# Kernel tuning notes

Hardware: AMD Instinct MI355X
Metric: run time of the kernel (lower is better)

The kernel has to match this reference:

```python
import jax, jax.numpy as jnp
import numpy as np


def setup_inputs() -> dict:
    key = jax.random.key(0)
    k1, k2, k3, k4, k5 = jax.random.split(key, 5)
    B, K, S, E, I, D = 4, 2, 512, 8, 1024, 2048
    x = jax.random.normal(k1, (B, S, I), dtype=jnp.float32)
    weights = jax.random.uniform(k2, (B, K, S), dtype=jnp.float32)
    ensembles = jax.random.randint(k3, (B, K, S), 0, E, dtype=jnp.int64)
    # xavier_uniform-style init for expert weight tables
    lim1 = float(np.sqrt(6.0 / (D + I)))
    proj_in = jax.random.uniform(k4, (E, D, I), dtype=jnp.float32, minval=-lim1, maxval=lim1)
    proj_out = jax.random.uniform(k5, (E, I, D), dtype=jnp.float32, minval=-lim1, maxval=lim1)
    return {"x": x, "weights": weights, "ensembles": ensembles,
            "proj_in": proj_in, "proj_out": proj_out}


def reference(x, weights, ensembles, proj_in, proj_out):
    # x: (B,S,I); weights/ensembles: (B,K,S); proj_in: (E,D,I); proj_out: (E,I,D)
    # Same math as the torch module (dropout = identity in eval):
    #   per token t, out = sum_k w[k,t] * W2[e_kt] @ relu(W1[e_kt] @ x[t])
    # Computed as all-expert batched GEMMs + a gated (one-hot scatter) combine,
    # which is mathematically identical and avoids the (B,K,S,D,I) gather blowup.
    E = proj_in.shape[0]
    h = jax.nn.relu(jnp.einsum('edi,bsi->bsed', proj_in, x))      # (B,S,E,D)
    o = jnp.einsum('eid,bsed->bsei', proj_out, h)                 # (B,S,E,I)
    onehot = jax.nn.one_hot(ensembles, E, dtype=x.dtype)          # (B,K,S,E)
    gate = jnp.einsum('bks,bkse->bse', weights, onehot)           # (B,S,E)
    return jnp.einsum('bsei,bse->bsi', o, gate)                   # (B,S,I)
```

## Files before the change

### kernel.cpp

```cpp
#include <hip/hip_runtime.h>
#include <stdint.h>

#define THREADS 512
#define BM 256
#define BN 128
#define BK 64
#define MAXT 24
#define NE 8
#define BB 4
#define SS 512
#define KK 2
#define II 1024
#define DD 2048
#define NTOK (BB * SS)
#define NASSIGN (BB * KK * SS)

#define CH_X (NTOK * II / 8)
#define CH_P (NE * DD * II / 8)
#define CB_X (CH_X / 256)
#define CB_P (CH_P / 256)
#define CB_TOTAL (CB_X + 2 * CB_P)

typedef unsigned short u16;
typedef __attribute__((ext_vector_type(8))) __bf16 bf16x8;
typedef __attribute__((ext_vector_type(4))) float f32x4;
typedef __attribute__((ext_vector_type(4))) unsigned int u32x4;

__device__ __forceinline__ u16 f32_to_bf16(float f) {
    unsigned int u = __builtin_bit_cast(unsigned int, f);
    unsigned int r = u + 0x7FFFu + ((u >> 16) & 1u);
    return (u16)(r >> 16);
}

__device__ __forceinline__ void gload16(const void* g, void* l) {
    __builtin_amdgcn_global_load_lds(
        (const __attribute__((address_space(1))) unsigned int*)g,
        (__attribute__((address_space(3))) unsigned int*)l, 16, 0, 0);
}

__global__ void setup_kernel(const void* __restrict__ ens_raw,
                             const float* __restrict__ weights,
                             int* __restrict__ meta,
                             int* __restrict__ tok,
                             float* __restrict__ wgt) {
    __shared__ int s_cnt[NE];
    __shared__ int s_cur[NE];
    __shared__ int s_flag;
    const int t = threadIdx.x;
    if (t < NE) s_cnt[t] = 0;
    if (t == 0) s_flag = 0;
    __syncthreads();

    const unsigned int* w32 = (const unsigned int*)ens_raw;
    unsigned int f = 0;
    for (int i = t; i < NASSIGN / 2; i += 256) f |= w32[2 * i + 1];
    if (f) atomicOr(&s_flag, 1);
    __syncthreads();
    const bool is32 = (s_flag != 0);
    const int* e32 = (const int*)ens_raw;
    const long long* e64 = (const long long*)ens_raw;

    for (int a = t; a < NASSIGN; a += 256) {
        int e = is32 ? e32[a] : (int)e64[a];
        atomicAdd(&s_cnt[e & 7], 1);
    }
    __syncthreads();

    if (t == 0) {
        int pb = 0, nt = 0;
        for (int e = 0; e < NE; e++) {
            int c = s_cnt[e];
            meta[8 + e] = c;
            meta[16 + e] = pb;
            s_cur[e] = pb;
            int n128 = (c + 127) >> 7;
            int pe = pb + n128 * 128;
            for (int i2 = 0; i2 < n128; i2 += 2) {
                meta[32 + nt] = e;
                meta[64 + nt] = pb + i2 * 128;
                meta[96 + nt] = pb + c;
                meta[128 + nt] = pe;
                nt++;
            }
            pb = pe;
        }
        meta[0] = nt;
        meta[1] = pb;
    }
    __syncthreads();

    for (int a = t; a < NASSIGN; a += 256) {
        int e = is32 ? e32[a] : (int)e64[a];
        e &= 7;
        int slot = atomicAdd(&s_cur[e], 1);
        int b = a >> 10;
        int s = a & (SS - 1);
        tok[slot] = b * SS + s;
        wgt[slot] = weights[a];
    }
    __syncthreads();

    for (int e = 0; e < NE; e++) {
        int st = meta[16 + e] + meta[8 + e];
        int en = (e < NE - 1) ? meta[16 + e + 1] : meta[1];
        for (int i = st + t; i < en; i += 256) {
            tok[i] = 0;
            wgt[i] = 0.f;
        }
    }
}

__global__ __launch_bounds__(256)
void convert3(const float* __restrict__ x,
              const float* __restrict__ pin,
              const float* __restrict__ pout,
              u16* __restrict__ xb,
              u16* __restrict__ pb1,
              u16* __restrict__ pb2) {
    const int b = blockIdx.x;
    const float* s;
    u16* d;
    int base;
    if (b < CB_X)            { s = x;    d = xb;  base = b << 8; }
    else if (b < CB_X + CB_P){ s = pin;  d = pb1; base = (b - CB_X) << 8; }
    else                     { s = pout; d = pb2; base = (b - CB_X - CB_P) << 8; }
    const size_t k = (size_t)base + threadIdx.x;
    const f32x4* s4 = (const f32x4*)s;
    f32x4 a = __builtin_nontemporal_load(&s4[2 * k]);
    f32x4 c = __builtin_nontemporal_load(&s4[2 * k + 1]);
    union { u16 u[8]; u32x4 v; } o;
    o.u[0] = f32_to_bf16(a[0]); o.u[1] = f32_to_bf16(a[1]);
    o.u[2] = f32_to_bf16(a[2]); o.u[3] = f32_to_bf16(a[3]);
    o.u[4] = f32_to_bf16(c[0]); o.u[5] = f32_to_bf16(c[1]);
    o.u[6] = f32_to_bf16(c[2]); o.u[7] = f32_to_bf16(c[3]);
    *(u32x4*)(d + 8 * k) = o.v;
}

template <int MODE>
__global__ __launch_bounds__(THREADS, 2)
void gemm256(const u16* __restrict__ Abase,
             const u16* __restrict__ Bbase,
             const int* __restrict__ meta,
             const int* __restrict__ tok,
             const float* __restrict__ wgt,
             u16* __restrict__ hdst,
             float* __restrict__ outdst) {
    constexpr int Kdim = (MODE == 0) ? II : DD;
    constexpr int NT = Kdim / BK;
    __shared__ char smem[3 * 49152];

    const int lid = blockIdx.x;
    const int g = lid & 7;
    const int i = lid >> 3;
    const int tile = g * 3 + (i % 3);
    const int colt = i / 3;
    if (tile >= meta[0]) return;

    const int e     = meta[32 + tile];
    const int sbase = meta[64 + tile];
    const int rend  = meta[96 + tile];
    const int wend  = meta[128 + tile];
    const int padmax = meta[1];
    const int colbase = colt * BN;

    const int tid = threadIdx.x;
    const int lane = tid & 63;
    const int wv = tid >> 6;
    const int wr = wv >> 1;
    const int wc = wv & 1;

    const u16* Bp = Bbase + (size_t)e * (size_t)(DD * II) + (size_t)colbase * Kdim;

    int aoff[4], boff[2], adst[4], bdst[2];
#pragma unroll
    for (int j = 0; j < 4; j++) {
        int c = j * 512 + tid;
        int row = c >> 3;
        int s = (c & 7) ^ (row & 7);
        adst[j] = c * 16;
        int slot = sbase + row;
        if (slot > padmax - 1) slot = padmax - 1;
        aoff[j] = (MODE == 0 ? tok[slot] * II : slot * DD) + s * 8;
    }
#pragma unroll
    for (int j = 0; j < 2; j++) {
        int c = j * 512 + tid;
        int row = c >> 3;
        int s = (c & 7) ^ (row & 7);
        bdst[j] = c * 16;
        boff[j] = row * Kdim + s * 8;
    }

    f32x4 acc[4][4];
#pragma unroll
    for (int m = 0; m < 4; m++)
#pragma unroll
        for (int n = 0; n < 4; n++)
            acc[m][n] = (f32x4){0.f, 0.f, 0.f, 0.f};

    auto STAGE = [&](int kt, char* buf) {
        const int kof = kt * BK;
#pragma unroll
        for (int j = 0; j < 4; j++)
            gload16(Abase + aoff[j] + kof, buf + adst[j]);
#pragma unroll
        for (int j = 0; j < 2; j++)
            gload16(Bp + boff[j] + kof, buf + 32768 + bdst[j]);
    };

    auto COMPUTE = [&](const char* buf) {
        const u16* As = (const u16*)buf;
        const u16* Bs = (const u16*)(buf + 32768);
        bf16x8 a[2][4], b[2][4];
#pragma unroll
        for (int kk = 0; kk < 2; kk++) {
#pragma unroll
            for (int m = 0; m < 4; m++) {
                int row = wr * 64 + m * 16 + (lane & 15);
                int slot = (kk * 4 + (lane >> 4)) ^ (row & 7);
                a[kk][m] = *(const bf16x8*)&As[row * 64 + slot * 8];
            }
#pragma unroll
            for (int n = 0; n < 4; n++) {
                int col = wc * 64 + n * 16 + (lane & 15);
                int slot = (kk * 4 + (lane >> 4)) ^ (col & 7);
                b[kk][n] = *(const bf16x8*)&Bs[col * 64 + slot * 8];
            }
        }
        __builtin_amdgcn_s_setprio(1);
#pragma unroll
        for (int m = 0; m < 4; m++)
#pragma unroll
            for (int n = 0; n < 4; n++) {
                acc[m][n] = __builtin_amdgcn_mfma_f32_16x16x32_bf16(
                    a[0][m], b[0][n], acc[m][n], 0, 0, 0);
                acc[m][n] = __builtin_amdgcn_mfma_f32_16x16x32_bf16(
                    a[1][m], b[1][n], acc[m][n], 0, 0, 0);
            }
        __builtin_amdgcn_s_setprio(0);
    };

    char* pA = smem;
    char* pB = smem + 49152;
    char* pC = smem + 98304;

    STAGE(0, pA);
    STAGE(1, pB);
    asm volatile("s_waitcnt vmcnt(6)" ::: "memory");
    __builtin_amdgcn_sched_barrier(0);
    __builtin_amdgcn_s_barrier();
    __builtin_amdgcn_sched_barrier(0);

#pragma unroll 1
    for (int t = 0; t < NT; ++t) {
        if (t + 2 < NT) STAGE(t + 2, pC);
        COMPUTE(pA);
        if (t + 2 < NT) {
            asm volatile("s_waitcnt vmcnt(6)" ::: "memory");
        } else if (t + 1 < NT) {
            asm volatile("s_waitcnt vmcnt(0)" ::: "memory");
        }
        __builtin_amdgcn_sched_barrier(0);
        __builtin_amdgcn_s_barrier();
        __builtin_amdgcn_sched_barrier(0);
        char* tmp = pA; pA = pB; pB = pC; pC = tmp;
    }

    if (MODE == 0) {
#pragma unroll
        for (int m = 0; m < 4; m++) {
#pragma unroll
            for (int r = 0; r < 4; r++) {
                int row = wr * 64 + m * 16 + (lane >> 4) * 4 + r;
                int slot = sbase + row;
                if (slot < wend) {
                    size_t ro = (size_t)slot * DD;
#pragma unroll
                    for (int n = 0; n < 4; n++) {
                        int col = colbase + wc * 64 + n * 16 + (lane & 15);
                        float v = acc[m][n][r];
                        v = v > 0.f ? v : 0.f;
                        hdst[ro + col] = f32_to_bf16(v);
                    }
                }
            }
        }
    } else {
#pragma unroll
        for (int m = 0; m < 4; m++) {
#pragma unroll
            for (int r = 0; r < 4; r++) {
                int row = wr * 64 + m * 16 + (lane >> 4) * 4 + r;
                int slot = sbase + row;
                if (slot < rend) {
                    float w = wgt[slot];
                    size_t obase = (size_t)tok[slot] * II;
#pragma unroll
                    for (int n = 0; n < 4; n++) {
                        int col = colbase + wc * 64 + n * 16 + (lane & 15);
                        atomicAdd(&outdst[obase + col], acc[m][n][r] * w);
                    }
                }
            }
        }
    }
}

extern "C" void kernel_launch(void* const* d_in, const int* in_sizes, int n_in,
                              void* d_out, int out_size, void* d_ws, size_t ws_size,
                              hipStream_t stream) {
    const float* x = (const float*)d_in[0];
    const float* weights = (const float*)d_in[1];
    const void* ens = d_in[2];
    const float* pin = (const float*)d_in[3];
    const float* pout = (const float*)d_in[4];
    float* out = (float*)d_out;

    char* ws = (char*)d_ws;
    int*   meta    = (int*)(ws);
    int*   tok     = (int*)(ws + 1024);
    float* wgt     = (float*)(ws + 21504);
    u16*   x_bf    = (u16*)(ws + 41984);
    u16*   pin_bf  = (u16*)(ws + 4236288);
    u16*   pout_bf = (u16*)(ws + 37790720);
    u16*   h       = (u16*)(ws + 71345152);

    setup_kernel<<<dim3(1), dim3(256), 0, stream>>>(ens, weights, meta, tok, wgt);

    hipMemsetAsync(d_out, 0, (size_t)out_size * sizeof(float), stream);

    convert3<<<dim3(CB_TOTAL), dim3(256), 0, stream>>>(x, pin, pout, x_bf, pin_bf, pout_bf);

    gemm256<0><<<dim3(8 * 3 * 16), dim3(THREADS), 0, stream>>>(
        x_bf, pin_bf, meta, tok, wgt, h, nullptr);

    gemm256<1><<<dim3(8 * 3 * 8), dim3(THREADS), 0, stream>>>(
        h, pout_bf, meta, tok, wgt, nullptr, out);
}
```

Baseline: 134.8 us.

## Fuse fp32-to-bf16 weight conversion into GEMM B-tile loads via registers

Drops the separate pass that converted both expert weight tables to bf16. The GEMMs now read the fp32 weights directly into registers, pack them with v_cvt_pk_bf16_f32, and write them into a double-buffered LDS B tile, with the main loop unrolled by two to alternate register sets. This removes a full read and write of about 134MB of weight data, but each GEMM block now fetches twice the bytes for B, and the same weight tile is re-read and re-converted by every tile that uses that expert. The tile-to-block mapping is also changed so that tiles for the same column share a block group.

```diff
diff --git a/kernel.cpp b/kernel.cpp
--- a/kernel.cpp
+++ b/kernel.cpp
@@ -5,7 +5,6 @@
 #define BM 256
 #define BN 128
 #define BK 64
-#define MAXT 24
 #define NE 8
 #define BB 4
 #define SS 512
@@ -16,10 +15,7 @@
 #define NASSIGN (BB * KK * SS)
 
 #define CH_X (NTOK * II / 8)
-#define CH_P (NE * DD * II / 8)
 #define CB_X (CH_X / 256)
-#define CB_P (CH_P / 256)
-#define CB_TOTAL (CB_X + 2 * CB_P)
 
 typedef unsigned short u16;
 typedef __attribute__((ext_vector_type(8))) __bf16 bf16x8;
@@ -32,11 +28,23 @@
     return (u16)(r >> 16);
 }
 
+__device__ __forceinline__ unsigned int cvtpk(float lo, float hi) {
+    unsigned int r;
+    asm("v_cvt_pk_bf16_f32 %0, %1, %2" : "=v"(r) : "v"(lo), "v"(hi));
+    return r;
+}
+
 __device__ __forceinline__ void gload16(const void* g, void* l) {
     __builtin_amdgcn_global_load_lds(
         (const __attribute__((address_space(1))) unsigned int*)g,
         (__attribute__((address_space(3))) unsigned int*)l, 16, 0, 0);
 }
+
+#define SYNC() do { \
+    asm volatile("s_waitcnt lgkmcnt(0)" ::: "memory"); \
+    __builtin_amdgcn_sched_barrier(0); \
+    __builtin_amdgcn_s_barrier(); \
+    __builtin_amdgcn_sched_barrier(0); } while (0)
 
 __global__ void setup_kernel(const void* __restrict__ ens_raw,
                              const float* __restrict__ weights,
@@ -111,21 +119,9 @@
 }
 
 __global__ __launch_bounds__(256)
-void convert3(const float* __restrict__ x,
-              const float* __restrict__ pin,
-              const float* __restrict__ pout,
-              u16* __restrict__ xb,
-              u16* __restrict__ pb1,
-              u16* __restrict__ pb2) {
-    const int b = blockIdx.x;
-    const float* s;
-    u16* d;
-    int base;
-    if (b < CB_X)            { s = x;    d = xb;  base = b << 8; }
-    else if (b < CB_X + CB_P){ s = pin;  d = pb1; base = (b - CB_X) << 8; }
-    else                     { s = pout; d = pb2; base = (b - CB_X - CB_P) << 8; }
-    const size_t k = (size_t)base + threadIdx.x;
-    const f32x4* s4 = (const f32x4*)s;
+void convertX(const float* __restrict__ x, u16* __restrict__ xb) {
+    const size_t k = (size_t)blockIdx.x * 256 + threadIdx.x;
+    const f32x4* s4 = (const f32x4*)x;
     f32x4 a = __builtin_nontemporal_load(&s4[2 * k]);
     f32x4 c = __builtin_nontemporal_load(&s4[2 * k + 1]);
     union { u16 u[8]; u32x4 v; } o;
@@ -133,13 +129,13 @@
     o.u[2] = f32_to_bf16(a[2]); o.u[3] = f32_to_bf16(a[3]);
     o.u[4] = f32_to_bf16(c[0]); o.u[5] = f32_to_bf16(c[1]);
     o.u[6] = f32_to_bf16(c[2]); o.u[7] = f32_to_bf16(c[3]);
-    *(u32x4*)(d + 8 * k) = o.v;
+    *(u32x4*)(xb + 8 * k) = o.v;
 }
 
 template <int MODE>
 __global__ __launch_bounds__(THREADS, 2)
 void gemm256(const u16* __restrict__ Abase,
-             const u16* __restrict__ Bbase,
+             const float* __restrict__ Bbase,
              const int* __restrict__ meta,
              const int* __restrict__ tok,
              const float* __restrict__ wgt,
@@ -147,19 +143,21 @@
              float* __restrict__ outdst) {
     constexpr int Kdim = (MODE == 0) ? II : DD;
     constexpr int NT = Kdim / BK;
-    __shared__ char smem[3 * 49152];
+    constexpr int ASZ = BM * BK * 2;
+    constexpr int BSZ = BN * BK * 2;
+    __shared__ char smem[3 * ASZ + 2 * BSZ];
 
     const int lid = blockIdx.x;
     const int g = lid & 7;
     const int i = lid >> 3;
-    const int tile = g * 3 + (i % 3);
+    const int tile = g + 8 * (i % 3);
     const int colt = i / 3;
     if (tile >= meta[0]) return;
 
-    const int e     = meta[32 + tile];
-    const int sbase = meta[64 + tile];
-    const int rend  = meta[96 + tile];
-    const int wend  = meta[128 + tile];
+    const int e      = meta[32 + tile];
+    const int sbase  = meta[64 + tile];
+    const int rend   = meta[96 + tile];
+    const int wend   = meta[128 + tile];
     const int padmax = meta[1];
     const int colbase = colt * BN;
 
@@ -169,9 +167,9 @@
     const int wr = wv >> 1;
     const int wc = wv & 1;
 
-    const u16* Bp = Bbase + (size_t)e * (size_t)(DD * II) + (size_t)colbase * Kdim;
-
-    int aoff[4], boff[2], adst[4], bdst[2];
+    const float* Bp32 = Bbase + (size_t)e * (size_t)(DD * II) + (size_t)colbase * Kdim;
+
+    int aoff[4], adst[4];
 #pragma unroll
     for (int j = 0; j < 4; j++) {
         int c = j * 512 + tid;
@@ -182,13 +180,15 @@
         if (slot > padmax - 1) slot = padmax - 1;
         aoff[j] = (MODE == 0 ? tok[slot] * II : slot * DD) + s * 8;
     }
+
+    int bsrc[2], bdst[2];
 #pragma unroll
     for (int j = 0; j < 2; j++) {
-        int c = j * 512 + tid;
-        int row = c >> 3;
-        int s = (c & 7) ^ (row & 7);
-        bdst[j] = c * 16;
-        boff[j] = row * Kdim + s * 8;
+        int c = 2 * tid + j;
+        int col = c >> 3;
+        int s0 = c & 7;
+        bsrc[j] = col * Kdim + s0 * 8;
+        bdst[j] = col * 128 + ((s0 ^ (col & 7)) * 16);
     }
 
     f32x4 acc[4][4];
@@ -198,19 +198,40 @@
         for (int n = 0; n < 4; n++)
             acc[m][n] = (f32x4){0.f, 0.f, 0.f, 0.f};
 
-    auto STAGE = [&](int kt, char* buf) {
+    f32x4 rE[2][2], rO[2][2];
+
+    auto STAGE_A = [&](int kt, char* buf) {
         const int kof = kt * BK;
 #pragma unroll
         for (int j = 0; j < 4; j++)
             gload16(Abase + aoff[j] + kof, buf + adst[j]);
-#pragma unroll
-        for (int j = 0; j < 2; j++)
-            gload16(Bp + boff[j] + kof, buf + 32768 + bdst[j]);
     };
 
-    auto COMPUTE = [&](const char* buf) {
-        const u16* As = (const u16*)buf;
-        const u16* Bs = (const u16*)(buf + 32768);
+    auto LOADB = [&](int kt, f32x4 (&R)[2][2]) {
+        const int kof = kt * BK;
+#pragma unroll
+        for (int j = 0; j < 2; j++) {
+            const f32x4* p = (const f32x4*)(Bp32 + bsrc[j] + kof);
+            R[j][0] = p[0];
+            R[j][1] = p[1];
+        }
+    };
+
+    auto WRITEB = [&](f32x4 (&R)[2][2], char* pbl) {
+#pragma unroll
+        for (int j = 0; j < 2; j++) {
+            u32x4 w;
+            w[0] = cvtpk(R[j][0][0], R[j][0][1]);
+            w[1] = cvtpk(R[j][0][2], R[j][0][3]);
+            w[2] = cvtpk(R[j][1][0], R[j][1][1]);
+            w[3] = cvtpk(R[j][1][2], R[j][1][3]);
+            *(u32x4*)(pbl + bdst[j]) = w;
+        }
+    };
+
+    auto COMPUTE = [&](const char* bufA, const char* bufB) {
+        const u16* As = (const u16*)bufA;
+        const u16* Bs = (const u16*)bufB;
         bf16x8 a[2][4], b[2][4];
 #pragma unroll
         for (int kk = 0; kk < 2; kk++) {
@@ -241,29 +262,31 @@
     };
 
     char* pA = smem;
-    char* pB = smem + 49152;
-    char* pC = smem + 98304;
-
-    STAGE(0, pA);
-    STAGE(1, pB);
-    asm volatile("s_waitcnt vmcnt(6)" ::: "memory");
+    char* pB = smem + ASZ;
+    char* pC = smem + 2 * ASZ;
+    char* pB0 = smem + 3 * ASZ;
+    char* pB1 = pB0 + BSZ;
+
+    STAGE_A(0, pA); LOADB(0, rE);
+    STAGE_A(1, pB); LOADB(1, rO);
     __builtin_amdgcn_sched_barrier(0);
-    __builtin_amdgcn_s_barrier();
-    __builtin_amdgcn_sched_barrier(0);
+    WRITEB(rE, pB0);
+    SYNC();
 
 #pragma unroll 1
-    for (int t = 0; t < NT; ++t) {
-        if (t + 2 < NT) STAGE(t + 2, pC);
-        COMPUTE(pA);
-        if (t + 2 < NT) {
-            asm volatile("s_waitcnt vmcnt(6)" ::: "memory");
-        } else if (t + 1 < NT) {
-            asm volatile("s_waitcnt vmcnt(0)" ::: "memory");
-        }
+    for (int t = 0; t < NT; t += 2) {
+        if (t + 2 < NT) { STAGE_A(t + 2, pC); LOADB(t + 2, rE); }
         __builtin_amdgcn_sched_barrier(0);
-        __builtin_amdgcn_s_barrier();
+        if (t + 1 < NT) WRITEB(rO, pB1);
+        COMPUTE(pA, pB0);
+        SYNC();
+        { char* tp = pA; pA = pB; pB = pC; pC = tp; }
+        if (t + 3 < NT) { STAGE_A(t + 3, pC); LOADB(t + 3, rO); }
         __builtin_amdgcn_sched_barrier(0);
-        char* tmp = pA; pA = pB; pB = pC; pC = tmp;
+        if (t + 2 < NT) WRITEB(rE, pB0);
+        COMPUTE(pA, pB1);
+        SYNC();
+        { char* tp = pA; pA = pB; pB = pC; pC = tp; }
     }
 
     if (MODE == 0) {
@@ -317,23 +340,21 @@
     float* out = (float*)d_out;
 
     char* ws = (char*)d_ws;
-    int*   meta    = (int*)(ws);
-    int*   tok     = (int*)(ws + 1024);
-    float* wgt     = (float*)(ws + 21504);
-    u16*   x_bf    = (u16*)(ws + 41984);
-    u16*   pin_bf  = (u16*)(ws + 4236288);
-    u16*   pout_bf = (u16*)(ws + 37790720);
-    u16*   h       = (u16*)(ws + 71345152);
+    int*   meta = (int*)(ws);
+    int*   tok  = (int*)(ws + 1024);
+    float* wgt  = (float*)(ws + 21504);
+    u16*   x_bf = (u16*)(ws + 41984);
+    u16*   h    = (u16*)(ws + 4236288);
 
     setup_kernel<<<dim3(1), dim3(256), 0, stream>>>(ens, weights, meta, tok, wgt);
 
     hipMemsetAsync(d_out, 0, (size_t)out_size * sizeof(float), stream);
 
-    convert3<<<dim3(CB_TOTAL), dim3(256), 0, stream>>>(x, pin, pout, x_bf, pin_bf, pout_bf);
+    convertX<<<dim3(CB_X), dim3(256), 0, stream>>>(x, x_bf);
 
     gemm256<0><<<dim3(8 * 3 * 16), dim3(THREADS), 0, stream>>>(
-        x_bf, pin_bf, meta, tok, wgt, h, nullptr);
+        x_bf, pin, meta, tok, wgt, h, nullptr);
 
     gemm256<1><<<dim3(8 * 3 * 8), dim3(THREADS), 0, stream>>>(
-        h, pout_bf, meta, tok, wgt, nullptr, out);
-}
+        h, pout, meta, tok, wgt, nullptr, out);
+}
```

Result: slower. 153.6 us (+14.0%).

## Split MFMA k-step into two phases with interleaved staged loads and barriers

Applied to the files above, without the earlier changes.

Splits each k-tile's compute into two half-M phases. Each phase reads its own LDS fragments, waits on lgkmcnt, then issues its MFMAs. Half of the next stage's global-to-LDS loads are issued before each phase, with an extra barrier between the phases, so memory traffic is spread through the compute and register pressure from fragments drops. The tile-to-block mapping also changes from g*3+i%3 to g+8*(i%3), which alters how expert tiles are spread across blocks. Risks include the extra barrier per iteration and loss of LDS-read/MFMA overlap caused by the explicit lgkmcnt(0) wait.

```diff
diff --git a/kernel.cpp b/kernel.cpp
--- a/kernel.cpp
+++ b/kernel.cpp
@@ -5,7 +5,6 @@
 #define BM 256
 #define BN 128
 #define BK 64
-#define MAXT 24
 #define NE 8
 #define BB 4
 #define SS 512
@@ -37,6 +36,11 @@
         (const __attribute__((address_space(1))) unsigned int*)g,
         (__attribute__((address_space(3))) unsigned int*)l, 16, 0, 0);
 }
+
+#define BARRIER() do { \
+    __builtin_amdgcn_sched_barrier(0); \
+    __builtin_amdgcn_s_barrier(); \
+    __builtin_amdgcn_sched_barrier(0); } while (0)
 
 __global__ void setup_kernel(const void* __restrict__ ens_raw,
                              const float* __restrict__ weights,
@@ -147,19 +151,20 @@
              float* __restrict__ outdst) {
     constexpr int Kdim = (MODE == 0) ? II : DD;
     constexpr int NT = Kdim / BK;
-    __shared__ char smem[3 * 49152];
+    constexpr int BUF = 49152;
+    __shared__ char smem[3 * BUF];
 
     const int lid = blockIdx.x;
     const int g = lid & 7;
     const int i = lid >> 3;
-    const int tile = g * 3 + (i % 3);
+    const int tile = g + 8 * (i % 3);
     const int colt = i / 3;
     if (tile >= meta[0]) return;
 
-    const int e     = meta[32 + tile];
-    const int sbase = meta[64 + tile];
-    const int rend  = meta[96 + tile];
-    const int wend  = meta[128 + tile];
+    const int e      = meta[32 + tile];
+    const int sbase  = meta[64 + tile];
+    const int rend   = meta[96 + tile];
+    const int wend   = meta[128 + tile];
     const int padmax = meta[1];
     const int colbase = colt * BN;
 
@@ -171,7 +176,7 @@
 
     const u16* Bp = Bbase + (size_t)e * (size_t)(DD * II) + (size_t)colbase * Kdim;
 
-    int aoff[4], boff[2], adst[4], bdst[2];
+    int aoff[4], adst[4], boff[2], bdst[2];
 #pragma unroll
     for (int j = 0; j < 4; j++) {
         int c = j * 512 + tid;
@@ -198,72 +203,80 @@
         for (int n = 0; n < 4; n++)
             acc[m][n] = (f32x4){0.f, 0.f, 0.f, 0.f};
 
-    auto STAGE = [&](int kt, char* buf) {
-        const int kof = kt * BK;
-#pragma unroll
-        for (int j = 0; j < 4; j++)
-            gload16(Abase + aoff[j] + kof, buf + adst[j]);
-#pragma unroll
-        for (int j = 0; j < 2; j++)
-            gload16(Bp + boff[j] + kof, buf + 32768 + bdst[j]);
-    };
-
-    auto COMPUTE = [&](const char* buf) {
+    auto PHASEM = [&](const char* buf, int qm) {
         const u16* As = (const u16*)buf;
         const u16* Bs = (const u16*)(buf + 32768);
-        bf16x8 a[2][4], b[2][4];
+        bf16x8 a[2][2], b[2][4];
 #pragma unroll
         for (int kk = 0; kk < 2; kk++) {
 #pragma unroll
-            for (int m = 0; m < 4; m++) {
-                int row = wr * 64 + m * 16 + (lane & 15);
+            for (int mi = 0; mi < 2; mi++) {
+                int row = wr * 64 + (qm * 2 + mi) * 16 + (lane & 15);
                 int slot = (kk * 4 + (lane >> 4)) ^ (row & 7);
-                a[kk][m] = *(const bf16x8*)&As[row * 64 + slot * 8];
-            }
-#pragma unroll
-            for (int n = 0; n < 4; n++) {
-                int col = wc * 64 + n * 16 + (lane & 15);
+                a[kk][mi] = *(const bf16x8*)&As[row * 64 + slot * 8];
+            }
+#pragma unroll
+            for (int ni = 0; ni < 4; ni++) {
+                int col = wc * 64 + ni * 16 + (lane & 15);
                 int slot = (kk * 4 + (lane >> 4)) ^ (col & 7);
-                b[kk][n] = *(const bf16x8*)&Bs[col * 64 + slot * 8];
-            }
-        }
+                b[kk][ni] = *(const bf16x8*)&Bs[col * 64 + slot * 8];
+            }
+        }
+        asm volatile("s_waitcnt lgkmcnt(0)" ::: "memory");
+        __builtin_amdgcn_sched_barrier(0);
         __builtin_amdgcn_s_setprio(1);
 #pragma unroll
-        for (int m = 0; m < 4; m++)
-#pragma unroll
-            for (int n = 0; n < 4; n++) {
-                acc[m][n] = __builtin_amdgcn_mfma_f32_16x16x32_bf16(
-                    a[0][m], b[0][n], acc[m][n], 0, 0, 0);
-                acc[m][n] = __builtin_amdgcn_mfma_f32_16x16x32_bf16(
-                    a[1][m], b[1][n], acc[m][n], 0, 0, 0);
+        for (int mi = 0; mi < 2; mi++)
+#pragma unroll
+            for (int ni = 0; ni < 4; ni++) {
+                int m = qm * 2 + mi;
+                acc[m][ni] = __builtin_amdgcn_mfma_f32_16x16x32_bf16(
+                    a[0][mi], b[0][ni], acc[m][ni], 0, 0, 0);
+                acc[m][ni] = __builtin_amdgcn_mfma_f32_16x16x32_bf16(
+                    a[1][mi], b[1][ni], acc[m][ni], 0, 0, 0);
             }
         __builtin_amdgcn_s_setprio(0);
     };
 
     char* pA = smem;
-    char* pB = smem + 49152;
-    char* pC = smem + 98304;
-
-    STAGE(0, pA);
-    STAGE(1, pB);
+    char* pB = smem + BUF;
+    char* pC = smem + 2 * BUF;
+
+#pragma unroll
+    for (int j = 0; j < 4; j++) gload16(Abase + aoff[j], pA + adst[j]);
+#pragma unroll
+    for (int j = 0; j < 2; j++) gload16(Bp + boff[j], pA + 32768 + bdst[j]);
+#pragma unroll
+    for (int j = 0; j < 4; j++) gload16(Abase + aoff[j] + BK, pB + adst[j]);
+#pragma unroll
+    for (int j = 0; j < 2; j++) gload16(Bp + boff[j] + BK, pB + 32768 + bdst[j]);
     asm volatile("s_waitcnt vmcnt(6)" ::: "memory");
-    __builtin_amdgcn_sched_barrier(0);
-    __builtin_amdgcn_s_barrier();
-    __builtin_amdgcn_sched_barrier(0);
+    BARRIER();
 
 #pragma unroll 1
     for (int t = 0; t < NT; ++t) {
-        if (t + 2 < NT) STAGE(t + 2, pC);
-        COMPUTE(pA);
-        if (t + 2 < NT) {
+        const bool st = (t + 2 < NT);
+        const int kof = (t + 2) * BK;
+        if (st) {
+            gload16(Abase + aoff[0] + kof, pC + adst[0]);
+            gload16(Abase + aoff[1] + kof, pC + adst[1]);
+            gload16(Bp + boff[0] + kof, pC + 32768 + bdst[0]);
+        }
+        PHASEM(pA, 0);
+        BARRIER();
+        if (st) {
+            gload16(Abase + aoff[2] + kof, pC + adst[2]);
+            gload16(Abase + aoff[3] + kof, pC + adst[3]);
+            gload16(Bp + boff[1] + kof, pC + 32768 + bdst[1]);
+        }
+        PHASEM(pA, 1);
+        if (st) {
             asm volatile("s_waitcnt vmcnt(6)" ::: "memory");
         } else if (t + 1 < NT) {
             asm volatile("s_waitcnt vmcnt(0)" ::: "memory");
         }
-        __builtin_amdgcn_sched_barrier(0);
-        __builtin_amdgcn_s_barrier();
-        __builtin_amdgcn_sched_barrier(0);
-        char* tmp = pA; pA = pB; pB = pC; pC = tmp;
+        BARRIER();
+        { char* tp = pA; pA = pB; pB = pC; pC = tp; }
     }
 
     if (MODE == 0) {
```

New measurement: 140.9 us. 4.6% more time.

## Halve K tile, split-K second GEMM, raise occupancy, fold setup into convert

Applied to the files above, without the earlier changes.

BK drops from 64 to 32, which shrinks the triple-buffered LDS footprint to 72KB. Launch bounds are raised to 4 blocks per SM so more workgroups fit per CU. The second GEMM is split along K into two halves via blockIdx.y, doubling its grid; this presumably depends on atomic accumulation into the zeroed output. The routing setup kernel is merged into the conversion kernel as an extra block, removing one launch, and the tile-to-block mapping is reordered. The risks are that the setup block now runs concurrently with the conversion blocks, extra register pressure from the tighter launch bounds, and more barriers per unit of work because the K tile is smaller.

```diff
diff --git a/kernel.cpp b/kernel.cpp
--- a/kernel.cpp
+++ b/kernel.cpp
@@ -4,8 +4,7 @@
 #define THREADS 512
 #define BM 256
 #define BN 128
-#define BK 64
-#define MAXT 24
+#define BK 32
 #define NE 8
 #define BB 4
 #define SS 512
@@ -38,11 +37,18 @@
         (__attribute__((address_space(3))) unsigned int*)l, 16, 0, 0);
 }
 
-__global__ void setup_kernel(const void* __restrict__ ens_raw,
-                             const float* __restrict__ weights,
-                             int* __restrict__ meta,
-                             int* __restrict__ tok,
-                             float* __restrict__ wgt) {
+#define BARRIER() do { \
+    __builtin_amdgcn_sched_barrier(0); \
+    __builtin_amdgcn_s_barrier(); \
+    __builtin_amdgcn_sched_barrier(0); } while (0)
+
+__device__ __forceinline__ int sw4(int row) { return (row ^ (row >> 2)) & 3; }
+
+__device__ void setup_body(const void* __restrict__ ens_raw,
+                           const float* __restrict__ weights,
+                           int* __restrict__ meta,
+                           int* __restrict__ tok,
+                           float* __restrict__ wgt) {
     __shared__ int s_cnt[NE];
     __shared__ int s_cur[NE];
     __shared__ int s_flag;
@@ -111,19 +117,28 @@
 }
 
 __global__ __launch_bounds__(256)
-void convert3(const float* __restrict__ x,
-              const float* __restrict__ pin,
-              const float* __restrict__ pout,
-              u16* __restrict__ xb,
-              u16* __restrict__ pb1,
-              u16* __restrict__ pb2) {
+void convert_setup(const float* __restrict__ x,
+                   const float* __restrict__ pin,
+                   const float* __restrict__ pout,
+                   u16* __restrict__ xb,
+                   u16* __restrict__ pb1,
+                   u16* __restrict__ pb2,
+                   const void* __restrict__ ens,
+                   const float* __restrict__ weights,
+                   int* __restrict__ meta,
+                   int* __restrict__ tok,
+                   float* __restrict__ wgt) {
     const int b = blockIdx.x;
+    if (b >= CB_TOTAL) {
+        setup_body(ens, weights, meta, tok, wgt);
+        return;
+    }
     const float* s;
     u16* d;
     int base;
-    if (b < CB_X)            { s = x;    d = xb;  base = b << 8; }
-    else if (b < CB_X + CB_P){ s = pin;  d = pb1; base = (b - CB_X) << 8; }
-    else                     { s = pout; d = pb2; base = (b - CB_X - CB_P) << 8; }
+    if (b < CB_X)             { s = x;    d = xb;  base = b << 8; }
+    else if (b < CB_X + CB_P) { s = pin;  d = pb1; base = (b - CB_X) << 8; }
+    else                      { s = pout; d = pb2; base = (b - CB_X - CB_P) << 8; }
     const size_t k = (size_t)base + threadIdx.x;
     const f32x4* s4 = (const f32x4*)s;
     f32x4 a = __builtin_nontemporal_load(&s4[2 * k]);
@@ -137,7 +152,7 @@
 }
 
 template <int MODE>
-__global__ __launch_bounds__(THREADS, 2)
+__global__ __launch_bounds__(THREADS, 4)
 void gemm256(const u16* __restrict__ Abase,
              const u16* __restrict__ Bbase,
              const int* __restrict__ meta,
@@ -146,22 +161,26 @@
              u16* __restrict__ hdst,
              float* __restrict__ outdst) {
     constexpr int Kdim = (MODE == 0) ? II : DD;
-    constexpr int NT = Kdim / BK;
-    __shared__ char smem[3 * 49152];
+    constexpr int NT = 32;
+    constexpr int ASZ = BM * BK * 2;
+    constexpr int BSZ = BN * BK * 2;
+    constexpr int BUFSZ = ASZ + BSZ;
+    __shared__ char smem[3 * BUFSZ];
 
     const int lid = blockIdx.x;
     const int g = lid & 7;
     const int i = lid >> 3;
-    const int tile = g * 3 + (i % 3);
+    const int tile = g + 8 * (i % 3);
     const int colt = i / 3;
     if (tile >= meta[0]) return;
 
-    const int e     = meta[32 + tile];
-    const int sbase = meta[64 + tile];
-    const int rend  = meta[96 + tile];
-    const int wend  = meta[128 + tile];
+    const int e      = meta[32 + tile];
+    const int sbase  = meta[64 + tile];
+    const int rend   = meta[96 + tile];
+    const int wend   = meta[128 + tile];
     const int padmax = meta[1];
     const int colbase = colt * BN;
+    const int kbase = (MODE == 1) ? blockIdx.y * 1024 : 0;
 
     const int tid = threadIdx.x;
     const int lane = tid & 63;
@@ -171,24 +190,22 @@
 
     const u16* Bp = Bbase + (size_t)e * (size_t)(DD * II) + (size_t)colbase * Kdim;
 
-    int aoff[4], boff[2], adst[4], bdst[2];
-#pragma unroll
-    for (int j = 0; j < 4; j++) {
+    int aoff[2], adst[2], boff, bdst;
+#pragma unroll
+    for (int j = 0; j < 2; j++) {
         int c = j * 512 + tid;
-        int row = c >> 3;
-        int s = (c & 7) ^ (row & 7);
+        int row = c >> 2;
+        int s = (c & 3) ^ sw4(row);
         adst[j] = c * 16;
         int slot = sbase + row;
         if (slot > padmax - 1) slot = padmax - 1;
-        aoff[j] = (MODE == 0 ? tok[slot] * II : slot * DD) + s * 8;
-    }
-#pragma unroll
-    for (int j = 0; j < 2; j++) {
-        int c = j * 512 + tid;
-        int row = c >> 3;
-        int s = (c & 7) ^ (row & 7);
-        bdst[j] = c * 16;
-        boff[j] = row * Kdim + s * 8;
+        aoff[j] = (MODE == 0 ? tok[slot] * II : slot * DD) + kbase + s * 8;
+    }
+    {
+        int col = tid >> 2;
+        int s = (tid & 3) ^ sw4(col);
+        bdst = tid * 16;
+        boff = col * Kdim + kbase + s * 8;
     }
 
     f32x4 acc[4][4];
@@ -200,70 +217,61 @@
 
     auto STAGE = [&](int kt, char* buf) {
         const int kof = kt * BK;
-#pragma unroll
-        for (int j = 0; j < 4; j++)
-            gload16(Abase + aoff[j] + kof, buf + adst[j]);
-#pragma unroll
-        for (int j = 0; j < 2; j++)
-            gload16(Bp + boff[j] + kof, buf + 32768 + bdst[j]);
+        gload16(Abase + aoff[0] + kof, buf + adst[0]);
+        gload16(Abase + aoff[1] + kof, buf + adst[1]);
+        gload16(Bp + boff + kof, buf + ASZ + bdst);
     };
 
     auto COMPUTE = [&](const char* buf) {
         const u16* As = (const u16*)buf;
-        const u16* Bs = (const u16*)(buf + 32768);
-        bf16x8 a[2][4], b[2][4];
-#pragma unroll
-        for (int kk = 0; kk < 2; kk++) {
-#pragma unroll
-            for (int m = 0; m < 4; m++) {
-                int row = wr * 64 + m * 16 + (lane & 15);
-                int slot = (kk * 4 + (lane >> 4)) ^ (row & 7);
-                a[kk][m] = *(const bf16x8*)&As[row * 64 + slot * 8];
-            }
-#pragma unroll
-            for (int n = 0; n < 4; n++) {
-                int col = wc * 64 + n * 16 + (lane & 15);
-                int slot = (kk * 4 + (lane >> 4)) ^ (col & 7);
-                b[kk][n] = *(const bf16x8*)&Bs[col * 64 + slot * 8];
-            }
-        }
+        const u16* Bs = (const u16*)(buf + ASZ);
+        bf16x8 a[4], b[4];
+        const int kseg = lane >> 4;
+#pragma unroll
+        for (int m = 0; m < 4; m++) {
+            int row = wr * 64 + m * 16 + (lane & 15);
+            int slotL = kseg ^ sw4(row);
+            a[m] = *(const bf16x8*)&As[row * BK + slotL * 8];
+        }
+#pragma unroll
+        for (int n = 0; n < 4; n++) {
+            int col = wc * 64 + n * 16 + (lane & 15);
+            int slotL = kseg ^ sw4(col);
+            b[n] = *(const bf16x8*)&Bs[col * BK + slotL * 8];
+        }
+        asm volatile("s_waitcnt lgkmcnt(0)" ::: "memory");
+        __builtin_amdgcn_sched_barrier(0);
         __builtin_amdgcn_s_setprio(1);
 #pragma unroll
         for (int m = 0; m < 4; m++)
 #pragma unroll
-            for (int n = 0; n < 4; n++) {
+            for (int n = 0; n < 4; n++)
                 acc[m][n] = __builtin_amdgcn_mfma_f32_16x16x32_bf16(
-                    a[0][m], b[0][n], acc[m][n], 0, 0, 0);
-                acc[m][n] = __builtin_amdgcn_mfma_f32_16x16x32_bf16(
-                    a[1][m], b[1][n], acc[m][n], 0, 0, 0);
-            }
+                    a[m], b[n], acc[m][n], 0, 0, 0);
         __builtin_amdgcn_s_setprio(0);
     };
 
     char* pA = smem;
-    char* pB = smem + 49152;
-    char* pC = smem + 98304;
+    char* pB = smem + BUFSZ;
+    char* pC = smem + 2 * BUFSZ;
 
     STAGE(0, pA);
     STAGE(1, pB);
-    asm volatile("s_waitcnt vmcnt(6)" ::: "memory");
-    __builtin_amdgcn_sched_barrier(0);
-    __builtin_amdgcn_s_barrier();
-    __builtin_amdgcn_sched_barrier(0);
+    asm volatile("s_waitcnt vmcnt(3)" ::: "memory");
+    BARRIER();
 
 #pragma unroll 1
     for (int t = 0; t < NT; ++t) {
-        if (t + 2 < NT) STAGE(t + 2, pC);
+        const bool st = (t + 2 < NT);
+        if (st) STAGE(t + 2, pC);
         COMPUTE(pA);
-        if (t + 2 < NT) {
-            asm volatile("s_waitcnt vmcnt(6)" ::: "memory");
+        if (st) {
+            asm volatile("s_waitcnt vmcnt(3)" ::: "memory");
         } else if (t + 1 < NT) {
             asm volatile("s_waitcnt vmcnt(0)" ::: "memory");
         }
-        __builtin_amdgcn_sched_barrier(0);
-        __builtin_amdgcn_s_barrier();
-        __builtin_amdgcn_sched_barrier(0);
-        char* tmp = pA; pA = pB; pB = pC; pC = tmp;
+        BARRIER();
+        { char* tp = pA; pA = pB; pB = pC; pC = tp; }
     }
 
     if (MODE == 0) {
@@ -325,15 +333,14 @@
     u16*   pout_bf = (u16*)(ws + 37790720);
     u16*   h       = (u16*)(ws + 71345152);
 
-    setup_kernel<<<dim3(1), dim3(256), 0, stream>>>(ens, weights, meta, tok, wgt);
-
     hipMemsetAsync(d_out, 0, (size_t)out_size * sizeof(float), stream);
 
-    convert3<<<dim3(CB_TOTAL), dim3(256), 0, stream>>>(x, pin, pout, x_bf, pin_bf, pout_bf);
+    convert_setup<<<dim3(CB_TOTAL + 1), dim3(256), 0, stream>>>(
+        x, pin, pout, x_bf, pin_bf, pout_bf, ens, weights, meta, tok, wgt);
 
     gemm256<0><<<dim3(8 * 3 * 16), dim3(THREADS), 0, stream>>>(
         x_bf, pin_bf, meta, tok, wgt, h, nullptr);
 
-    gemm256<1><<<dim3(8 * 3 * 8), dim3(THREADS), 0, stream>>>(
+    gemm256<1><<<dim3(8 * 3 * 8, 2), dim3(THREADS), 0, stream>>>(
         h, pout_bf, meta, tok, wgt, nullptr, out);
 }
```

Measured after the change: 142.0 us. 5.3% more time.
